# Kernel tuning notes

Hardware: AMD Instinct MI355X
Metric: run time of the kernel (lower is better)

Reference implementation:

```python
import jax, jax.numpy as jnp
import numpy as np


def conv3x3(x, w, b):
    # stride 1, pad 1, NCHW / OIHW
    out = jax.lax.conv_general_dilated(x, w, (1, 1), ((1, 1), (1, 1)),
                                       dimension_numbers=('NCHW', 'OIHW', 'NCHW'))
    return out + b[None, :, None, None]


def bilinear_sample(x, ys, xs):
    # x: [B,C,H,W]; ys,xs: [B,K,H,W] float sampling coords.
    # mmcv-style: zero outside image, per-corner validity.
    B, C, H, W = x.shape
    x_flat = x.reshape(B, C, H * W)
    y0 = jnp.floor(ys)
    x0 = jnp.floor(xs)
    dy = ys - y0
    dx = xs - x0
    y0i = y0.astype(jnp.int32)
    x0i = x0.astype(jnp.int32)

    def corner(yc, xc, wgt):
        valid = (yc >= 0) & (yc < H) & (xc >= 0) & (xc < W)
        idx = jnp.clip(yc, 0, H - 1) * W + jnp.clip(xc, 0, W - 1)  # [B,K,H,W]
        idx_f = idx.reshape(B, -1)
        vals = jax.vmap(lambda xf, ix: xf[:, ix])(x_flat, idx_f)  # [B,C,K*H*W]
        vals = vals.reshape(B, C, *yc.shape[1:])
        return vals * (wgt * valid)[:, None]

    out = corner(y0i, x0i, (1 - dy) * (1 - dx))
    out = out + corner(y0i, x0i + 1, (1 - dy) * dx)
    out = out + corner(y0i + 1, x0i, dy * (1 - dx))
    out = out + corner(y0i + 1, x0i + 1, dy * dx)
    return out  # [B,C,K,H,W]


def avgpool3s2(z):
    # AvgPool2d(kernel=3, stride=2, padding=1), count_include_pad=True -> divide by 9
    s = jax.lax.reduce_window(z, 0.0, jax.lax.add, (1, 1, 3, 3), (1, 1, 2, 2),
                              ((0, 0), (0, 0), (1, 1), (1, 1)))
    return s / 9.0


def setup_inputs() -> dict:
    key = jax.random.key(0)
    k1, k2, k3 = jax.random.split(key, 3)
    C = 64
    x = jax.random.normal(k1, (4, C, 128, 128), dtype=jnp.float32)
    w_off = jax.random.normal(k2, (27, C, 3, 3), dtype=jnp.float32) * 0.02
    b_off = jnp.zeros((27,), dtype=jnp.float32)
    w_align = jax.random.normal(k3, (C, C, 3, 3), dtype=jnp.float32) * 0.02
    b_align = jnp.zeros((C,), dtype=jnp.float32)
    return {"x": x, "w_off": w_off, "b_off": b_off, "w_align": w_align, "b_align": b_align}


def reference(x, w_off, b_off, w_align, b_align):
    B, C, H, W = x.shape
    K = 9
    off_all = conv3x3(x, w_off, b_off)               # [B,27,H,W]
    offset = off_all[:, :2 * K]                      # [B,18,H,W]
    mask = 2.0 * jax.nn.sigmoid(off_all[:, 2 * K:])  # [B,9,H,W]
    off = offset.reshape(B, K, 2, H, W)
    dy = off[:, :, 0]
    dx = off[:, :, 1]
    # base kernel grid (dilation 1, pad 1): offsets in {-1,0,1}
    ky = (jnp.arange(K) // 3 - 1).astype(jnp.float32)
    kx = (jnp.arange(K) % 3 - 1).astype(jnp.float32)
    ys = jnp.arange(H, dtype=jnp.float32)[None, None, :, None] + ky[None, :, None, None] + dy
    xs = jnp.arange(W, dtype=jnp.float32)[None, None, None, :] + kx[None, :, None, None] + dx
    sampled = bilinear_sample(x, ys, xs) * mask[:, None]    # [B,C,K,H,W]
    w = jnp.einsum('bckhw,ock->bohw', sampled, w_align.reshape(C, C, K))
    w = w + b_align[None, :, None, None]
    w = jnp.exp(jax.nn.sigmoid(w))
    return avgpool3s2(w * x) / avgpool3s2(w)
```

## Files before the change

### kernel.cpp

```cpp
#include <hip/hip_runtime.h>
#include <hip/hip_bf16.h>

#define HW 16384
#define CC 64
#define BB 4

typedef __attribute__((ext_vector_type(8))) short bf8;
typedef __attribute__((ext_vector_type(4))) float f4;

static __device__ __forceinline__ float bf2f(unsigned short u) {
    return __uint_as_float(((unsigned)u) << 16);
}
static __device__ __forceinline__ unsigned short f2bf(float f) {
    __hip_bfloat16 h = __float2bfloat16(f);
    return *reinterpret_cast<unsigned short*>(&h);
}

__global__ __launch_bounds__(256) void k_prep_tx(const float* __restrict__ x,
                                                 const float* __restrict__ w_off,
                                                 const float* __restrict__ w_align,
                                                 unsigned short* __restrict__ xT,
                                                 unsigned short* __restrict__ wA,
                                                 unsigned short* __restrict__ Wal2) {
    __shared__ unsigned T32[64 * 33];
    int bx = blockIdx.x, t = threadIdx.x;
    if (bx < 216) {
        int i = bx * 256 + t;
        if (i < 32 * 576) {
            int m = i / 576, r = i - m * 576, tt = r >> 6, c = r & 63;
            float v = (m < 27) ? w_off[m * 576 + c * 9 + tt] : 0.f;
            wA[i] = f2bf(v);
        } else {
            int j = i - 32 * 576;
            int jj = j & 7;
            int chunk = j >> 3;
            int l = chunk & 63;
            int g = chunk >> 6;
            int mt = g & 3;
            int th = g >> 2;
            int h2 = th & 1;
            int tp = th >> 1;
            int o = mt * 16 + (l & 15);
            int c = h2 * 32 + (l >> 4) * 8 + jj;
            Wal2[j] = f2bf(w_align[o * 576 + c * 9 + tp]);
        }
        return;
    }
    int pix0 = (bx - 216) * 64;
    int b = pix0 >> 14, hw0 = pix0 & (HW - 1);
    const float* xb = x + (size_t)b * CC * HW + hw0;
#pragma unroll
    for (int u = 0; u < 8; u++) {
        int i = t + 256 * u;
        int cp = i >> 6, p = i & 63;
        float v0 = xb[(size_t)(2 * cp) * HW + p];
        float v1 = xb[(size_t)(2 * cp + 1) * HW + p];
        T32[p * 33 + cp] = (unsigned)f2bf(v0) | ((unsigned)f2bf(v1) << 16);
    }
    __syncthreads();
#pragma unroll
    for (int u = 0; u < 2; u++) {
        int i = t + 256 * u;
        int p = i >> 3, q = i & 7;
        uint4 qq;
        qq.x = T32[p * 33 + q * 4 + 0];
        qq.y = T32[p * 33 + q * 4 + 1];
        qq.z = T32[p * 33 + q * 4 + 2];
        qq.w = T32[p * 33 + q * 4 + 3];
        *(uint4*)(xT + ((size_t)b * HW + hw0 + p) * CC + q * 8) = qq;
    }
}

__global__ __launch_bounds__(256, 4) void k_conv(const unsigned short* __restrict__ xT,
                                                 const unsigned short* __restrict__ wA,
                                                 const float* __restrict__ b_off,
                                                 float* __restrict__ off) {
    __shared__ __align__(16) unsigned short WL[32 * 584];
    int t = threadIdx.x, lane = t & 63, wv = t >> 6;
    int quad = lane >> 4, col = lane & 15;
#pragma unroll
    for (int u = 0; u < 9; u++) {
        int idx = t + 256 * u;
        int row = idx / 72, jb = idx - row * 72;
        *(uint4*)(WL + row * 584 + jb * 8) = ((const uint4*)wA)[idx];
    }
    __syncthreads();

    int n = blockIdx.x * 64 + wv * 16 + col;
    int b = n >> 14, hw = n & (HW - 1), h = hw >> 7, w = hw & 127;
    const unsigned short* xTb = xT + (size_t)b * HW * CC;
    const bf8 zero = {0, 0, 0, 0, 0, 0, 0, 0};

    f4 acc0 = {0.f, 0.f, 0.f, 0.f};
    f4 acc1 = {0.f, 0.f, 0.f, 0.f};
#pragma unroll
    for (int tap = 0; tap < 9; tap++) {
        int dyt = tap / 3 - 1, dxt = tap - (tap / 3) * 3 - 1;
        int hs = h + dyt, ws = w + dxt;
        bool valid = ((unsigned)hs < 128u) && ((unsigned)ws < 128u);
        int hc = min(max(hs, 0), 127), wc = min(max(ws, 0), 127);
        const unsigned short* src = xTb + ((size_t)(hc * 128 + wc)) * CC + quad * 8;
        bf8 b0 = *(const bf8*)(src);
        bf8 b1 = *(const bf8*)(src + 32);
        b0 = valid ? b0 : zero;
        b1 = valid ? b1 : zero;
        const unsigned short* l0 = WL + col * 584 + tap * 64 + quad * 8;
        const unsigned short* l1 = WL + (col + 16) * 584 + tap * 64 + quad * 8;
        acc0 = __builtin_amdgcn_mfma_f32_16x16x32_bf16(*(const bf8*)l0, b0, acc0, 0, 0, 0);
        acc1 = __builtin_amdgcn_mfma_f32_16x16x32_bf16(*(const bf8*)l1, b0, acc1, 0, 0, 0);
        acc0 = __builtin_amdgcn_mfma_f32_16x16x32_bf16(*(const bf8*)(l0 + 32), b1, acc0, 0, 0, 0);
        acc1 = __builtin_amdgcn_mfma_f32_16x16x32_bf16(*(const bf8*)(l1 + 32), b1, acc1, 0, 0, 0);
    }
#pragma unroll
    for (int i = 0; i < 4; i++) {
        int o0 = quad * 4 + i;
        {
            float v = acc0[i] + b_off[o0];
            if (o0 >= 18) v = 2.f / (1.f + __expf(-v));
            off[((size_t)b * 27 + o0) * HW + hw] = v;
        }
        int o1 = 16 + o0;
        if (o1 < 27) {
            float v = acc1[i] + b_off[o1];
            if (o1 >= 18) v = 2.f / (1.f + __expf(-v));
            off[((size_t)b * 27 + o1) * HW + hw] = v;
        }
    }
}

__global__ __launch_bounds__(256, 4) void k_fused(const unsigned short* __restrict__ xT,
                                                  const float* __restrict__ off,
                                                  const unsigned short* __restrict__ Wal2,
                                                  const float* __restrict__ b_align,
                                                  float* __restrict__ wten) {
    int t = threadIdx.x, lane = t & 63, wv = t >> 6;
    int quad = lane >> 4, col = lane & 15;
    int pix0 = blockIdx.x * 64;
    int b = pix0 >> 14;
    int px = (pix0 & (HW - 1)) + wv * 16 + col;
    int h = px >> 7, w = px & 127;
    const unsigned short* xTb = xT + (size_t)b * HW * CC;
    const float* offp = off + (size_t)b * 27 * HW + px;
    const unsigned short* wl = Wal2 + lane * 8;

    float dyv[9], dxv[9], mv[9];
#pragma unroll
    for (int k = 0; k < 9; k++) {
        dyv[k] = offp[(size_t)(2 * k) * HW];
        dxv[k] = offp[(size_t)(2 * k + 1) * HW];
        mv[k]  = offp[(size_t)(18 + k) * HW];
    }

    f4 acc[4];
#pragma unroll
    for (int mt = 0; mt < 4; mt++) acc[mt] = (f4){0.f, 0.f, 0.f, 0.f};

#pragma unroll
    for (int k = 0; k < 9; k++) {
        float dy = dyv[k], dx = dxv[k], m = mv[k];
        int k3 = k / 3;
        float ys = (float)(h + k3 - 1) + dy;
        float xs = (float)(w + (k - 3 * k3) - 1) + dx;
        float y0f = floorf(ys), x0f = floorf(xs);
        float fy = ys - y0f, fx = xs - x0f;
        int y0 = (int)y0f, x0 = (int)x0f;
        int y1 = y0 + 1, x1 = x0 + 1;
        bool vy0 = (unsigned)y0 < 128u, vy1 = (unsigned)y1 < 128u;
        bool vx0 = (unsigned)x0 < 128u, vx1 = (unsigned)x1 < 128u;
        int cy0 = min(max(y0, 0), 127), cy1 = min(max(y1, 0), 127);
        int cx0 = min(max(x0, 0), 127), cx1 = min(max(x1, 0), 127);
        float w00 = (1.f - fy) * (1.f - fx) * ((vy0 && vx0) ? m : 0.f);
        float w01 = (1.f - fy) * fx         * ((vy0 && vx1) ? m : 0.f);
        float w10 = fy * (1.f - fx)         * ((vy1 && vx0) ? m : 0.f);
        float w11 = fy * fx                 * ((vy1 && vx1) ? m : 0.f);

        const unsigned short* c00 = xTb + ((size_t)(cy0 * 128 + cx0)) * CC + quad * 8;
        const unsigned short* c01 = xTb + ((size_t)(cy0 * 128 + cx1)) * CC + quad * 8;
        const unsigned short* c10 = xTb + ((size_t)(cy1 * 128 + cx0)) * CC + quad * 8;
        const unsigned short* c11 = xTb + ((size_t)(cy1 * 128 + cx1)) * CC + quad * 8;
        uint4 qa0 = *(const uint4*)(c00),      qa1 = *(const uint4*)(c01);
        uint4 qa2 = *(const uint4*)(c10),      qa3 = *(const uint4*)(c11);
        uint4 qb0 = *(const uint4*)(c00 + 32), qb1 = *(const uint4*)(c01 + 32);
        uint4 qb2 = *(const uint4*)(c10 + 32), qb3 = *(const uint4*)(c11 + 32);

        bf8 bfrag[2];
#pragma unroll
        for (int h2 = 0; h2 < 2; h2++) {
            const unsigned short* u00 = (const unsigned short*)(h2 ? &qb0 : &qa0);
            const unsigned short* u01 = (const unsigned short*)(h2 ? &qb1 : &qa1);
            const unsigned short* u10 = (const unsigned short*)(h2 ? &qb2 : &qa2);
            const unsigned short* u11 = (const unsigned short*)(h2 ? &qb3 : &qa3);
            unsigned short ov[8];
#pragma unroll
            for (int j = 0; j < 8; j++) {
                float v = w00 * bf2f(u00[j]) + w01 * bf2f(u01[j])
                        + w10 * bf2f(u10[j]) + w11 * bf2f(u11[j]);
                ov[j] = f2bf(v);
            }
            bfrag[h2] = *(const bf8*)ov;
        }
#pragma unroll
        for (int h2 = 0; h2 < 2; h2++) {
#pragma unroll
            for (int mt = 0; mt < 4; mt++) {
                const bf8 a = *(const bf8*)(wl + (size_t)(((k * 2 + h2) * 4 + mt) * 512));
                acc[mt] = __builtin_amdgcn_mfma_f32_16x16x32_bf16(a, bfrag[h2], acc[mt], 0, 0, 0);
            }
        }
    }

    float* wb = wten + (size_t)b * CC * HW + px;
#pragma unroll
    for (int mt = 0; mt < 4; mt++)
#pragma unroll
        for (int i = 0; i < 4; i++) {
            int o = mt * 16 + quad * 4 + i;
            float u = acc[mt][i] + b_align[o];
            float sg = 1.f / (1.f + __expf(-u));
            wb[(size_t)o * HW] = __expf(sg);
        }
}

__global__ __launch_bounds__(256) void k_pool(const float* __restrict__ x,
                                              const float* __restrict__ wten,
                                              float* __restrict__ out) {
    int idx = blockIdx.x * 256 + threadIdx.x;
    int ow = idx & 63;
    int oh = (idx >> 6) & 63;
    int bc = idx >> 12;
    const float* wp = wten + (size_t)bc * HW;
    const float* xp = x + (size_t)bc * HW;
    float num = 0.f, den = 0.f;
#pragma unroll
    for (int iy = 0; iy < 3; iy++) {
        int y = 2 * oh + iy - 1;
        if ((unsigned)y >= 128u) continue;
#pragma unroll
        for (int ix = 0; ix < 3; ix++) {
            int xc = 2 * ow + ix - 1;
            if ((unsigned)xc >= 128u) continue;
            float wv = wp[y * 128 + xc];
            float xv = xp[y * 128 + xc];
            num = fmaf(wv, xv, num);
            den += wv;
        }
    }
    out[idx] = num / den;
}

extern "C" void kernel_launch(void* const* d_in, const int* in_sizes, int n_in,
                              void* d_out, int out_size, void* d_ws, size_t ws_size,
                              hipStream_t stream) {
    const float* x       = (const float*)d_in[0];
    const float* w_off   = (const float*)d_in[1];
    const float* b_off   = (const float*)d_in[2];
    const float* w_align = (const float*)d_in[3];
    const float* b_align = (const float*)d_in[4];
    float* out = (float*)d_out;

    char* p = (char*)d_ws;
    float* off  = (float*)p;                  p += (size_t)BB * 27 * HW * 4;
    float* wten = (float*)p;                  p += (size_t)BB * CC * HW * 4;
    unsigned short* xT  = (unsigned short*)p; p += (size_t)BB * HW * CC * 2;
    unsigned short* wA  = (unsigned short*)p; p += 32 * 576 * 2;
    unsigned short* Wal2 = (unsigned short*)p;

    k_prep_tx<<<dim3(1240), dim3(256), 0, stream>>>(x, w_off, w_align, xT, wA, Wal2);
    k_conv<<<dim3(1024), dim3(256), 0, stream>>>(xT, wA, b_off, off);
    k_fused<<<dim3(1024), dim3(256), 0, stream>>>(xT, off, Wal2, b_align, wten);
    k_pool<<<dim3(4096), dim3(256), 0, stream>>>(x, wten, out);
}
```

Measured before the change: 135.9 us.

## Stage input halo tiles in LDS for conv and deformable sampling kernels

The offset conv kernel now loads a swizzled 3x66-pixel halo tile of the transposed input into shared memory and reads its taps from there. Its weights move from an LDS copy to a pre-swizzled global layout read directly as MFMA fragments. The deformable kernel stages a 6x70-pixel halo tile in LDS, reads bilinear corners from it when they fall inside, and falls back to global loads otherwise. Its occupancy hint drops to 3 blocks per CU to make room for the ~53KB tile, trading occupancy and staging cost for fewer scattered global/L2 reads.

After: 117.0 us. 1.16x faster.

```diff
diff --git a/kernel.cpp b/kernel.cpp
--- a/kernel.cpp
+++ b/kernel.cpp
@@ -20,16 +20,24 @@
                                                  const float* __restrict__ w_off,
                                                  const float* __restrict__ w_align,
                                                  unsigned short* __restrict__ xT,
-                                                 unsigned short* __restrict__ wA,
+                                                 unsigned short* __restrict__ wA2,
                                                  unsigned short* __restrict__ Wal2) {
     __shared__ unsigned T32[64 * 33];
     int bx = blockIdx.x, t = threadIdx.x;
     if (bx < 216) {
         int i = bx * 256 + t;
         if (i < 32 * 576) {
-            int m = i / 576, r = i - m * 576, tt = r >> 6, c = r & 63;
-            float v = (m < 27) ? w_off[m * 576 + c * 9 + tt] : 0.f;
-            wA[i] = f2bf(v);
+            int jj = i & 7;
+            int chunk = i >> 3;
+            int l = chunk & 63;
+            int g = chunk >> 6;
+            int m2 = g & 1;
+            int h2 = (g >> 1) & 1;
+            int tp = g >> 2;
+            int m = m2 * 16 + (l & 15);
+            int c = h2 * 32 + (l >> 4) * 8 + jj;
+            float v = (m < 27) ? w_off[m * 576 + c * 9 + tp] : 0.f;
+            wA2[i] = f2bf(v);
         } else {
             int j = i - 32 * 576;
             int jj = j & 7;
@@ -72,25 +80,35 @@
 }
 
 __global__ __launch_bounds__(256, 4) void k_conv(const unsigned short* __restrict__ xT,
-                                                 const unsigned short* __restrict__ wA,
+                                                 const unsigned short* __restrict__ wA2,
                                                  const float* __restrict__ b_off,
                                                  float* __restrict__ off) {
-    __shared__ __align__(16) unsigned short WL[32 * 584];
+    __shared__ __align__(16) unsigned short TC[198 * 64];
     int t = threadIdx.x, lane = t & 63, wv = t >> 6;
     int quad = lane >> 4, col = lane & 15;
-#pragma unroll
-    for (int u = 0; u < 9; u++) {
-        int idx = t + 256 * u;
-        int row = idx / 72, jb = idx - row * 72;
-        *(uint4*)(WL + row * 584 + jb * 8) = ((const uint4*)wA)[idx];
+    int n0 = blockIdx.x * 64;
+    int b = n0 >> 14, hw0 = n0 & (HW - 1);
+    int h = hw0 >> 7, w0 = hw0 & 127;
+    int pxo = wv * 16 + col;
+    int hw = hw0 + pxo, w = w0 + pxo;
+    const unsigned short* xTb = xT + (size_t)b * HW * CC;
+
+#pragma unroll
+    for (int u = 0; u < 7; u++) {
+        int i = t + 256 * u;
+        if (i < 1584) {
+            int e = i >> 3, s = i & 7;
+            int ty = e / 66, tx = e - ty * 66;
+            int gy = min(max(h - 1 + ty, 0), 127);
+            int gx = min(max(w0 - 1 + tx, 0), 127);
+            int c = s ^ (e & 7);
+            uint4 q = *(const uint4*)(xTb + ((size_t)((gy << 7) + gx)) * CC + c * 8);
+            *(uint4*)(TC + i * 8) = q;
+        }
     }
     __syncthreads();
 
-    int n = blockIdx.x * 64 + wv * 16 + col;
-    int b = n >> 14, hw = n & (HW - 1), h = hw >> 7, w = hw & 127;
-    const unsigned short* xTb = xT + (size_t)b * HW * CC;
     const bf8 zero = {0, 0, 0, 0, 0, 0, 0, 0};
-
     f4 acc0 = {0.f, 0.f, 0.f, 0.f};
     f4 acc1 = {0.f, 0.f, 0.f, 0.f};
 #pragma unroll
@@ -98,18 +116,20 @@
         int dyt = tap / 3 - 1, dxt = tap - (tap / 3) * 3 - 1;
         int hs = h + dyt, ws = w + dxt;
         bool valid = ((unsigned)hs < 128u) && ((unsigned)ws < 128u);
-        int hc = min(max(hs, 0), 127), wc = min(max(ws, 0), 127);
-        const unsigned short* src = xTb + ((size_t)(hc * 128 + wc)) * CC + quad * 8;
-        bf8 b0 = *(const bf8*)(src);
-        bf8 b1 = *(const bf8*)(src + 32);
+        int e = (dyt + 1) * 66 + pxo + dxt + 1;
+        int sL = quad ^ (e & 7);
+        bf8 b0 = *(const bf8*)(TC + e * 64 + (sL << 3));
+        bf8 b1 = *(const bf8*)(TC + e * 64 + ((sL ^ 4) << 3));
         b0 = valid ? b0 : zero;
         b1 = valid ? b1 : zero;
-        const unsigned short* l0 = WL + col * 584 + tap * 64 + quad * 8;
-        const unsigned short* l1 = WL + (col + 16) * 584 + tap * 64 + quad * 8;
-        acc0 = __builtin_amdgcn_mfma_f32_16x16x32_bf16(*(const bf8*)l0, b0, acc0, 0, 0, 0);
-        acc1 = __builtin_amdgcn_mfma_f32_16x16x32_bf16(*(const bf8*)l1, b0, acc1, 0, 0, 0);
-        acc0 = __builtin_amdgcn_mfma_f32_16x16x32_bf16(*(const bf8*)(l0 + 32), b1, acc0, 0, 0, 0);
-        acc1 = __builtin_amdgcn_mfma_f32_16x16x32_bf16(*(const bf8*)(l1 + 32), b1, acc1, 0, 0, 0);
+        const bf8 a00 = *(const bf8*)(wA2 + (((tap * 4 + 0) * 64 + lane) << 3));
+        const bf8 a01 = *(const bf8*)(wA2 + (((tap * 4 + 1) * 64 + lane) << 3));
+        const bf8 a10 = *(const bf8*)(wA2 + (((tap * 4 + 2) * 64 + lane) << 3));
+        const bf8 a11 = *(const bf8*)(wA2 + (((tap * 4 + 3) * 64 + lane) << 3));
+        acc0 = __builtin_amdgcn_mfma_f32_16x16x32_bf16(a00, b0, acc0, 0, 0, 0);
+        acc1 = __builtin_amdgcn_mfma_f32_16x16x32_bf16(a01, b0, acc1, 0, 0, 0);
+        acc0 = __builtin_amdgcn_mfma_f32_16x16x32_bf16(a10, b1, acc0, 0, 0, 0);
+        acc1 = __builtin_amdgcn_mfma_f32_16x16x32_bf16(a11, b1, acc1, 0, 0, 0);
     }
 #pragma unroll
     for (int i = 0; i < 4; i++) {
@@ -128,17 +148,20 @@
     }
 }
 
-__global__ __launch_bounds__(256, 4) void k_fused(const unsigned short* __restrict__ xT,
+__global__ __launch_bounds__(256, 3) void k_fused(const unsigned short* __restrict__ xT,
                                                   const float* __restrict__ off,
                                                   const unsigned short* __restrict__ Wal2,
                                                   const float* __restrict__ b_align,
                                                   float* __restrict__ wten) {
+    __shared__ __align__(16) unsigned short TF[420 * 64];
+
     int t = threadIdx.x, lane = t & 63, wv = t >> 6;
     int quad = lane >> 4, col = lane & 15;
     int pix0 = blockIdx.x * 64;
-    int b = pix0 >> 14;
-    int px = (pix0 & (HW - 1)) + wv * 16 + col;
-    int h = px >> 7, w = px & 127;
+    int b = pix0 >> 14, hw0 = pix0 & (HW - 1);
+    int h = hw0 >> 7, w0 = hw0 & 127;
+    int pxo = wv * 16 + col;
+    int px = hw0 + pxo, w = w0 + pxo;
     const unsigned short* xTb = xT + (size_t)b * HW * CC;
     const float* offp = off + (size_t)b * 27 * HW + px;
     const unsigned short* wl = Wal2 + lane * 8;
@@ -150,6 +173,23 @@
         dxv[k] = offp[(size_t)(2 * k + 1) * HW];
         mv[k]  = offp[(size_t)(18 + k) * HW];
     }
+
+#pragma unroll
+    for (int u = 0; u < 14; u++) {
+        int i = t + 256 * u;
+        if (i < 3360) {
+            int e = i >> 3, s = i & 7;
+            int ty = e / 70, tx = e - ty * 70;
+            int gy = min(max(h - 2 + ty, 0), 127);
+            int gx = min(max(w0 - 3 + tx, 0), 127);
+            int c = s ^ (e & 7);
+            uint4 q = *(const uint4*)(xTb + ((size_t)((gy << 7) + gx)) * CC + c * 8);
+            *(uint4*)(TF + i * 8) = q;
+        }
+    }
+    __syncthreads();
+
+    int hm2 = h - 2, hp3 = h + 3, wm3 = w0 - 3, wp66 = w0 + 66;
 
     f4 acc[4];
 #pragma unroll
@@ -174,14 +214,31 @@
         float w10 = fy * (1.f - fx)         * ((vy1 && vx0) ? m : 0.f);
         float w11 = fy * fx                 * ((vy1 && vx1) ? m : 0.f);
 
-        const unsigned short* c00 = xTb + ((size_t)(cy0 * 128 + cx0)) * CC + quad * 8;
-        const unsigned short* c01 = xTb + ((size_t)(cy0 * 128 + cx1)) * CC + quad * 8;
-        const unsigned short* c10 = xTb + ((size_t)(cy1 * 128 + cx0)) * CC + quad * 8;
-        const unsigned short* c11 = xTb + ((size_t)(cy1 * 128 + cx1)) * CC + quad * 8;
-        uint4 qa0 = *(const uint4*)(c00),      qa1 = *(const uint4*)(c01);
-        uint4 qa2 = *(const uint4*)(c10),      qa3 = *(const uint4*)(c11);
-        uint4 qb0 = *(const uint4*)(c00 + 32), qb1 = *(const uint4*)(c01 + 32);
-        uint4 qb2 = *(const uint4*)(c10 + 32), qb3 = *(const uint4*)(c11 + 32);
+        bool inT = (cy0 >= hm2) & (cy1 <= hp3) & (cx0 >= wm3) & (cx1 <= wp66);
+        uint4 qa0, qa1, qa2, qa3, qb0, qb1, qb2, qb3;
+        if (inT) {
+            int r0 = (cy0 - hm2) * 70 - wm3, r1 = (cy1 - hm2) * 70 - wm3;
+            int e00 = r0 + cx0, e01 = r0 + cx1, e10 = r1 + cx0, e11 = r1 + cx1;
+            int s00 = quad ^ (e00 & 7), s01 = quad ^ (e01 & 7);
+            int s10 = quad ^ (e10 & 7), s11 = quad ^ (e11 & 7);
+            qa0 = *(const uint4*)(TF + e00 * 64 + (s00 << 3));
+            qa1 = *(const uint4*)(TF + e01 * 64 + (s01 << 3));
+            qa2 = *(const uint4*)(TF + e10 * 64 + (s10 << 3));
+            qa3 = *(const uint4*)(TF + e11 * 64 + (s11 << 3));
+            qb0 = *(const uint4*)(TF + e00 * 64 + ((s00 ^ 4) << 3));
+            qb1 = *(const uint4*)(TF + e01 * 64 + ((s01 ^ 4) << 3));
+            qb2 = *(const uint4*)(TF + e10 * 64 + ((s10 ^ 4) << 3));
+            qb3 = *(const uint4*)(TF + e11 * 64 + ((s11 ^ 4) << 3));
+        } else {
+            const unsigned short* c00 = xTb + ((size_t)(cy0 * 128 + cx0)) * CC + quad * 8;
+            const unsigned short* c01 = xTb + ((size_t)(cy0 * 128 + cx1)) * CC + quad * 8;
+            const unsigned short* c10 = xTb + ((size_t)(cy1 * 128 + cx0)) * CC + quad * 8;
+            const unsigned short* c11 = xTb + ((size_t)(cy1 * 128 + cx1)) * CC + quad * 8;
+            qa0 = *(const uint4*)(c00);      qa1 = *(const uint4*)(c01);
+            qa2 = *(const uint4*)(c10);      qa3 = *(const uint4*)(c11);
+            qb0 = *(const uint4*)(c00 + 32); qb1 = *(const uint4*)(c01 + 32);
+            qb2 = *(const uint4*)(c10 + 32); qb3 = *(const uint4*)(c11 + 32);
+        }
 
         bf8 bfrag[2];
 #pragma unroll
@@ -262,11 +319,11 @@
     float* off  = (float*)p;                  p += (size_t)BB * 27 * HW * 4;
     float* wten = (float*)p;                  p += (size_t)BB * CC * HW * 4;
     unsigned short* xT  = (unsigned short*)p; p += (size_t)BB * HW * CC * 2;
-    unsigned short* wA  = (unsigned short*)p; p += 32 * 576 * 2;
+    unsigned short* wA2 = (unsigned short*)p; p += 32 * 576 * 2;
     unsigned short* Wal2 = (unsigned short*)p;
 
-    k_prep_tx<<<dim3(1240), dim3(256), 0, stream>>>(x, w_off, w_align, xT, wA, Wal2);
-    k_conv<<<dim3(1024), dim3(256), 0, stream>>>(xT, wA, b_off, off);
+    k_prep_tx<<<dim3(1240), dim3(256), 0, stream>>>(x, w_off, w_align, xT, wA2, Wal2);
+    k_conv<<<dim3(1024), dim3(256), 0, stream>>>(xT, wA2, b_off, off);
     k_fused<<<dim3(1024), dim3(256), 0, stream>>>(xT, off, Wal2, b_align, wten);
     k_pool<<<dim3(4096), dim3(256), 0, stream>>>(x, wten, out);
 }
```
